# Optimization experiments

Hardware: AMD Instinct MI355X
Metric: run time of the kernel (lower is better)

## Reference

```python
import jax, jax.numpy as jnp
import numpy as np

N_NODES = 100000
N_EDGES = 100000
NNZ = 3200000
D_IN, D_HID, N_CLS = 512, 16, 7
NEG_SLOPE = 0.2


def _segment_softmax(scores, seg, num_segments, sorted_seg):
    m = jax.ops.segment_max(scores, seg, num_segments=num_segments,
                            indices_are_sorted=sorted_seg)
    ex = jnp.exp(scores - m[seg])
    s = jax.ops.segment_sum(ex, seg, num_segments=num_segments,
                            indices_are_sorted=sorted_seg)
    return ex / (s[seg] + 1e-9)


def _hypergat_layer(X, W, a1, a2, node_idx, edge_idx):
    # X: [N, din] -> h: [N, dout]
    h = X @ W
    hv = h[node_idx]                                   # [nnz, dout] gather
    # phase 1: node -> hyperedge attention (softmax within each hyperedge)
    s1 = jax.nn.leaky_relu(hv @ a1, NEG_SLOPE)         # [nnz]
    alpha = _segment_softmax(s1, edge_idx, N_EDGES, True)
    e = jax.ops.segment_sum(alpha[:, None] * hv, edge_idx,
                            num_segments=N_EDGES, indices_are_sorted=True)
    # phase 2: hyperedge -> node attention (softmax over edges incident to node)
    ev = e[edge_idx]                                   # [nnz, dout] gather
    s2 = jax.nn.leaky_relu(jnp.concatenate([hv, ev], axis=-1) @ a2, NEG_SLOPE)
    beta = _segment_softmax(s2, node_idx, N_NODES, False)
    out = jax.ops.segment_sum(beta[:, None] * ev, node_idx,
                              num_segments=N_NODES)
    return out


def setup_inputs() -> dict:
    key = jax.random.key(0)
    ks = jax.random.split(key, 8)
    H = jax.random.normal(ks[0], (N_NODES, D_IN), dtype=jnp.float32)
    node_idx = jax.random.randint(ks[1], (NNZ,), 0, N_NODES)
    edge_idx = jnp.sort(jax.random.randint(ks[2], (NNZ,), 0, N_EDGES))
    g1 = 1.0 / np.sqrt(D_IN)
    g2 = 1.0 / np.sqrt(D_HID)
    W1 = jax.random.uniform(ks[3], (D_IN, D_HID), jnp.float32, -g1, g1)
    a1_1 = jax.random.uniform(ks[4], (D_HID,), jnp.float32, -g2, g2)
    a2_1 = jax.random.uniform(ks[5], (2 * D_HID,), jnp.float32, -g2, g2)
    W2 = jax.random.uniform(ks[6], (D_HID, N_CLS), jnp.float32, -g2, g2)
    k7, k8 = jax.random.split(ks[7])
    gc = 1.0 / np.sqrt(N_CLS)
    a1_2 = jax.random.uniform(k7, (N_CLS,), jnp.float32, -gc, gc)
    a2_2 = jax.random.uniform(k8, (2 * N_CLS,), jnp.float32, -gc, gc)
    return {"H": H, "W1": W1, "a1_1": a1_1, "a2_1": a2_1,
            "W2": W2, "a1_2": a1_2, "a2_2": a2_2,
            "node_idx": node_idx, "edge_idx": edge_idx}


def reference(H, W1, a1_1, a2_1, W2, a1_2, a2_2, node_idx, edge_idx):
    H1 = _hypergat_layer(H, W1, a1_1, a2_1, node_idx, edge_idx)   # [N, 16]
    X2 = jax.nn.elu(H1)                                           # dropout off (eval)
    H2 = _hypergat_layer(X2, W2, a1_2, a2_2, node_idx, edge_idx)  # [N, 7]
    logp = jax.nn.log_softmax(H2, axis=1)
    return (logp, H1, H2)
```

## Files before the change

kernel.cpp:

```cpp
#include <hip/hip_runtime.h>
#include <hip/hip_bf16.h>
#include <math.h>

#define N_NODES 100000
#define N_EDGESC 100000
#define NNZ_C   3200000
#define D_IN    512
#define D_HID   16
#define N_CLS   7
#define NBK     782

#define G_GEMM 1563
#define G_HIST 1000
#define G_EOFF 3125
#define G_BIN  1000

typedef short short8 __attribute__((ext_vector_type(8)));
typedef float f32x4  __attribute__((ext_vector_type(4)));

__device__ __forceinline__ unsigned short f2bf_rn(float x) {
  unsigned int u = __float_as_uint(x);
  u += 0x7fff + ((u >> 16) & 1);
  return (unsigned short)(u >> 16);
}
__device__ __forceinline__ float bf2f(unsigned short b) {
  return __uint_as_float(((unsigned int)b) << 16);
}

__device__ __forceinline__ void eoff_body(int b, const int* __restrict__ eidx,
                                          int* __restrict__ eoff) {
  int i0 = (b * 256 + threadIdx.x) * 4;
  if (i0 >= NNZ_C) return;
  int4 v4 = *(const int4*)(eidx + i0);
  int vv[4] = {v4.x, v4.y, v4.z, v4.w};
  int prev = (i0 == 0) ? -1 : eidx[i0 - 1];
#pragma unroll
  for (int k = 0; k < 4; ++k) {
    for (int e = prev + 1; e <= vv[k]; ++e) eoff[e] = i0 + k;
    prev = vv[k];
  }
  if (i0 + 4 == NNZ_C) {
    for (int e = prev + 1; e <= N_EDGESC; ++e) eoff[e] = NNZ_C;
  }
}

__device__ __forceinline__ void hist_body(int b, const int* __restrict__ nidx,
                                          int* __restrict__ gcnt) {
  __shared__ int lh[NBK];
  int t = threadIdx.x;
  for (int i = t; i < NBK; i += 256) lh[i] = 0;
  __syncthreads();
  int base = b * 3200, end = base + 3200;
  for (int i = base + t; i < end; i += 256) atomicAdd(&lh[nidx[i] >> 7], 1);
  __syncthreads();
  for (int i = t; i < NBK; i += 256) {
    int c = lh[i];
    if (c) atomicAdd(&gcnt[i], c);
  }
}

__device__ __forceinline__ void bin_body(int b, const int* __restrict__ nidx,
                                         const int* __restrict__ eidx,
                                         int* __restrict__ bcur, int* __restrict__ binned) {
  __shared__ int lh[NBK];
  __shared__ int gb[NBK];
  int t = threadIdx.x;
  for (int i = t; i < NBK; i += 256) lh[i] = 0;
  __syncthreads();
  int base = b * 3200, end = base + 3200;
  for (int i = base + t; i < end; i += 256) atomicAdd(&lh[nidx[i] >> 7], 1);
  __syncthreads();
  for (int i = t; i < NBK; i += 256) {
    int c = lh[i];
    gb[i] = c ? atomicAdd(&bcur[i], c) : 0;
    lh[i] = 0;
  }
  __syncthreads();
  for (int i = base + t; i < end; i += 256) {
    int v = nidx[i], e = eidx[i];
    int bk = v >> 7;
    int r = atomicAdd(&lh[bk], 1);
    binned[gb[bk] + r] = e | ((v & 127) << 20);
  }
}

__global__ void bscan_kernel(const int* __restrict__ gcnt, int* __restrict__ boff,
                             int* __restrict__ bcur) {
  __shared__ int lds[1024];
  int t = threadIdx.x;
  int v = (t < NBK) ? gcnt[t] : 0;
  lds[t] = v;
  __syncthreads();
  for (int d = 1; d < 1024; d <<= 1) {
    int u = (t >= d) ? lds[t - d] : 0;
    __syncthreads();
    lds[t] += u;
    __syncthreads();
  }
  if (t < NBK) {
    boff[t + 1] = lds[t];
    bcur[t] = lds[t] - v;
  }
  if (t == 0) boff[0] = 0;
}

__global__ void csr_kernel(const int* __restrict__ binned, const int* __restrict__ boff,
                           int* __restrict__ noff, int* __restrict__ perm_e, int N) {
  __shared__ int lh[128];
  __shared__ int lsc[128];
  __shared__ int lcur[128];
  int b = blockIdx.x;
  int t = threadIdx.x;
  int s = boff[b], e = boff[b + 1];
  if (t < 128) lh[t] = 0;
  __syncthreads();
  for (int i = s + t; i < e; i += 256) {
    atomicAdd(&lh[binned[i] >> 20], 1);
  }
  __syncthreads();
  if (t < 128) lsc[t] = lh[t];
  __syncthreads();
  for (int d = 1; d < 128; d <<= 1) {
    int u = (t < 128 && t >= d) ? lsc[t - d] : 0;
    __syncthreads();
    if (t < 128) lsc[t] += u;
    __syncthreads();
  }
  if (t < 128) {
    int excl = lsc[t] - lh[t];
    lcur[t] = excl;
    int n = b * 128 + t;
    if (n <= N) noff[n] = s + excl;
  }
  __syncthreads();
  for (int i = s + t; i < e; i += 256) {
    int p = binned[i];
    int r = atomicAdd(&lcur[p >> 20], 1);
    perm_e[s + r] = p & 0xFFFFF;
  }
}

__device__ __forceinline__ void gemm1_body(int b,
    const float* __restrict__ X, const float* __restrict__ W,
    const float* __restrict__ a1, const float* __restrict__ a2,
    float* __restrict__ Hout, float2* __restrict__ phv) {
  int wid = b * 4 + (threadIdx.x >> 6);
  if (wid >= 6250) return;
  int lane = threadIdx.x & 63;
  int col  = lane & 15;
  int quad = lane >> 4;

  short8 wh[16], wl[16];
#pragma unroll
  for (int c = 0; c < 16; ++c) {
#pragma unroll
    for (int j = 0; j < 8; ++j) {
      float w = W[(c * 32 + quad * 8 + j) * 16 + col];
      unsigned short h = f2bf_rn(w);
      wh[c][j] = (short)h;
      wl[c][j] = (short)f2bf_rn(w - bf2f(h));
    }
  }

  int rowbase = wid * 16;
  const float4* Xr = (const float4*)(X + (size_t)(rowbase + col) * D_IN) + quad * 2;

  f32x4 acc_hh = {0.f, 0.f, 0.f, 0.f};
  f32x4 acc_hl = {0.f, 0.f, 0.f, 0.f};
  f32x4 acc_lh = {0.f, 0.f, 0.f, 0.f};

  float4 pre[4][2];
#pragma unroll
  for (int q = 0; q < 4; ++q) { pre[q][0] = Xr[q * 8]; pre[q][1] = Xr[q * 8 + 1]; }
#pragma unroll
  for (int c = 0; c < 16; ++c) {
    float4 u0 = pre[c & 3][0], u1 = pre[c & 3][1];
    if (c < 12) { pre[c & 3][0] = Xr[(c + 4) * 8]; pre[c & 3][1] = Xr[(c + 4) * 8 + 1]; }
    float xs[8] = {u0.x, u0.y, u0.z, u0.w, u1.x, u1.y, u1.z, u1.w};
    short8 ah, al;
#pragma unroll
    for (int j = 0; j < 8; ++j) {
      unsigned short h = f2bf_rn(xs[j]);
      ah[j] = (short)h;
      al[j] = (short)f2bf_rn(xs[j] - bf2f(h));
    }
    acc_hh = __builtin_amdgcn_mfma_f32_16x16x32_bf16(ah, wh[c], acc_hh, 0, 0, 0);
    acc_hl = __builtin_amdgcn_mfma_f32_16x16x32_bf16(ah, wl[c], acc_hl, 0, 0, 0);
    acc_lh = __builtin_amdgcn_mfma_f32_16x16x32_bf16(al, wh[c], acc_lh, 0, 0, 0);
  }

  float a1c = a1[col], a2c = a2[col];
#pragma unroll
  for (int r = 0; r < 4; ++r) {
    float v = acc_hh[r] + acc_hl[r] + acc_lh[r];
    int row = rowbase + quad * 4 + r;
    Hout[(size_t)row * 16 + col] = v;
    float p1 = v * a1c, p2 = v * a2c;
#pragma unroll
    for (int d = 1; d < 16; d <<= 1) { p1 += __shfl_xor(p1, d); p2 += __shfl_xor(p2, d); }
    if (col == 0) phv[row] = make_float2(p1, p2);
  }
}

__global__ __launch_bounds__(256) void k1_kernel(
    const float* __restrict__ X, const float* __restrict__ W1,
    const float* __restrict__ a1_1, const float* __restrict__ a2_1,
    float* __restrict__ Hout, float2* __restrict__ phv,
    const int* __restrict__ eidx, int* __restrict__ eoff,
    const int* __restrict__ nidx, int* __restrict__ gcnt) {
  int b = blockIdx.x;
  if (b < G_GEMM) {
    gemm1_body(b, X, W1, a1_1, a2_1, Hout, phv);
  } else if (b < G_GEMM + G_HIST) {
    hist_body(b - G_GEMM, nidx, gcnt);
  } else {
    eoff_body(b - G_GEMM - G_HIST, eidx, eoff);
  }
}

__device__ __forceinline__ void edge1_body(
    const float* __restrict__ h, const float2* __restrict__ phv,
    const float* __restrict__ a2, const int* __restrict__ eoff,
    const int* __restrict__ nidx, float* __restrict__ eout,
    float* __restrict__ pe, int wave, int lane) {
  if (wave >= N_EDGESC) return;
  int o0 = eoff[wave], o1 = eoff[wave + 1];
  int g = lane >> 4, t = lane & 15;
  if (o0 == o1) {
    if (g == 0) {
      eout[(size_t)wave * 16 + t] = 0.f;
      if (t == 0) pe[wave] = 0.f;
    }
    return;
  }
  float m = -1e30f, l = 0.f, acc = 0.f;
  for (int base = o0; base < o1; base += 64) {
    int nrem = o1 - base; if (nrem > 64) nrem = 64;
    int li = base + lane;
    int idx_l = nidx[li < o1 ? li : o1 - 1];
    for (int jb = 0; jb < nrem; jb += 16) {
      int j = jb + g;
      bool ok0 = j < nrem, ok1 = j + 4 < nrem, ok2 = j + 8 < nrem, ok3 = j + 12 < nrem;
      int v0 = __shfl(idx_l, j);
      int v1 = __shfl(idx_l, j + 4);
      int v2 = __shfl(idx_l, j + 8);
      int v3 = __shfl(idx_l, j + 12);
      float P0 = phv[v0].x, P1 = phv[v1].x, P2 = phv[v2].x, P3 = phv[v3].x;
      float h0 = h[(size_t)v0 * 16 + t];
      float h1 = h[(size_t)v1 * 16 + t];
      float h2 = h[(size_t)v2 * 16 + t];
      float h3 = h[(size_t)v3 * 16 + t];
      float s0 = ok0 ? (P0 > 0.f ? P0 : 0.2f * P0) : -1e30f;
      float s1 = ok1 ? (P1 > 0.f ? P1 : 0.2f * P1) : -1e30f;
      float s2 = ok2 ? (P2 > 0.f ? P2 : 0.2f * P2) : -1e30f;
      float s3 = ok3 ? (P3 > 0.f ? P3 : 0.2f * P3) : -1e30f;
      float mn = fmaxf(fmaxf(m, fmaxf(s0, s1)), fmaxf(s2, s3));
      float eo = __expf(m - mn);
      float e0 = ok0 ? __expf(s0 - mn) : 0.f;
      float e1 = ok1 ? __expf(s1 - mn) : 0.f;
      float e2 = ok2 ? __expf(s2 - mn) : 0.f;
      float e3 = ok3 ? __expf(s3 - mn) : 0.f;
      l = l * eo + ((e0 + e1) + (e2 + e3));
      acc = acc * eo + ((e0 * h0 + e1 * h1) + (e2 * h2 + e3 * h3));
      m = mn;
    }
  }
#pragma unroll
  for (int d = 16; d < 64; d <<= 1) {
    float mo = __shfl_xor(m, d), lo = __shfl_xor(l, d), ao = __shfl_xor(acc, d);
    float mn = fmaxf(m, mo);
    float ea = __expf(m - mn), eb = __expf(mo - mn);
    l = l * ea + lo * eb;
    acc = acc * ea + ao * eb;
    m = mn;
  }
  float val = acc / (l + 1e-9f);
  float pav = val * a2[16 + t];
#pragma unroll
  for (int d = 1; d < 16; d <<= 1) pav += __shfl_xor(pav, d);
  if (g == 0) {
    eout[(size_t)wave * 16 + t] = val;
    if (t == 0) pe[wave] = pav;
  }
}

__global__ __launch_bounds__(256) void k3_kernel(
    const int* __restrict__ nidx, const int* __restrict__ eidx,
    int* __restrict__ bcur, int* __restrict__ binned,
    const float* __restrict__ h1g, const float2* __restrict__ phv,
    const float* __restrict__ a2_1, const int* __restrict__ eoff,
    float* __restrict__ e1, float* __restrict__ pe) {
  int b = blockIdx.x;
  if (b < G_BIN) {
    bin_body(b, nidx, eidx, bcur, binned);
  } else {
    int wave = (b - G_BIN) * 4 + (threadIdx.x >> 6);
    edge1_body(h1g, phv, a2_1, eoff, nidx, e1, pe, wave, threadIdx.x & 63);
  }
}

__global__ __launch_bounds__(256) void node1_kernel(
    const float2* __restrict__ phv, const float* __restrict__ e1,
    const float* __restrict__ pe, const int* __restrict__ noff,
    const int* __restrict__ perm_e, float* __restrict__ H1out,
    float* __restrict__ h2g8, const float* __restrict__ W2,
    const float* __restrict__ a1_2, const float* __restrict__ a2_2,
    float* __restrict__ pn2) {
  int wave = (blockIdx.x * blockDim.x + threadIdx.x) >> 6;
  int lane = threadIdx.x & 63;
  if (wave >= N_NODES) return;
  int o0 = noff[wave], o1 = noff[wave + 1];
  int g = lane >> 4, t = lane & 15;
  float ph = phv[wave].y;
  float m = -1e30f, l = 0.f, acc = 0.f;
  for (int base = o0; base < o1; base += 64) {
    int nrem = o1 - base; if (nrem > 64) nrem = 64;
    int li = base + lane;
    int idx_l = perm_e[li < o1 ? li : o1 - 1];
    for (int jb = 0; jb < nrem; jb += 16) {
      int j = jb + g;
      bool ok0 = j < nrem, ok1 = j + 4 < nrem, ok2 = j + 8 < nrem, ok3 = j + 12 < nrem;
      int E0 = __shfl(idx_l, j);
      int E1 = __shfl(idx_l, j + 4);
      int E2 = __shfl(idx_l, j + 8);
      int E3 = __shfl(idx_l, j + 12);
      float P0 = ph + pe[E0], P1 = ph + pe[E1], P2 = ph + pe[E2], P3 = ph + pe[E3];
      float h0 = e1[(size_t)E0 * 16 + t];
      float h1 = e1[(size_t)E1 * 16 + t];
      float h2 = e1[(size_t)E2 * 16 + t];
      float h3 = e1[(size_t)E3 * 16 + t];
      float s0 = ok0 ? (P0 > 0.f ? P0 : 0.2f * P0) : -1e30f;
      float s1 = ok1 ? (P1 > 0.f ? P1 : 0.2f * P1) : -1e30f;
      float s2 = ok2 ? (P2 > 0.f ? P2 : 0.2f * P2) : -1e30f;
      float s3 = ok3 ? (P3 > 0.f ? P3 : 0.2f * P3) : -1e30f;
      float mn = fmaxf(fmaxf(m, fmaxf(s0, s1)), fmaxf(s2, s3));
      float eo = __expf(m - mn);
      float e0 = ok0 ? __expf(s0 - mn) : 0.f;
      float e1x = ok1 ? __expf(s1 - mn) : 0.f;
      float e2x = ok2 ? __expf(s2 - mn) : 0.f;
      float e3x = ok3 ? __expf(s3 - mn) : 0.f;
      l = l * eo + ((e0 + e1x) + (e2x + e3x));
      acc = acc * eo + ((e0 * h0 + e1x * h1) + (e2x * h2 + e3x * h3));
      m = mn;
    }
  }
#pragma unroll
  for (int d = 16; d < 64; d <<= 1) {
    float mo = __shfl_xor(m, d), lo = __shfl_xor(l, d), ao = __shfl_xor(acc, d);
    float ea_, eb_;
    float mn = fmaxf(m, mo);
    ea_ = __expf(m - mn); eb_ = __expf(mo - mn);
    l = l * ea_ + lo * eb_;
    acc = acc * ea_ + ao * eb_;
    m = mn;
  }
  float val = acc / (l + 1e-9f);
  if (g == 0) H1out[(size_t)wave * 16 + t] = val;
  float x = val > 0.f ? val : expm1f(val);
  float p1 = 0.f, p2s = 0.f, myh2 = 0.f;
#pragma unroll
  for (int j = 0; j < N_CLS; ++j) {
    float term = x * W2[t * N_CLS + j];
#pragma unroll
    for (int d = 1; d < 16; d <<= 1) term += __shfl_xor(term, d);
    p1 += term * a1_2[j];
    p2s += term * a2_2[j];
    if (t == j) myh2 = term;
  }
  if (g == 0) {
    if (t < N_CLS) h2g8[(size_t)wave * 8 + t] = myh2;
    if (t == 7) h2g8[(size_t)wave * 8 + 7] = p1;
    if (t == 0) pn2[wave] = p2s;
  }
}

__global__ __launch_bounds__(256) void edge2_kernel(
    const float* __restrict__ h2g8, const int* __restrict__ eoff,
    const int* __restrict__ nidx, const float* __restrict__ a2_2,
    float* __restrict__ e28) {
  int wave = (blockIdx.x * blockDim.x + threadIdx.x) >> 6;
  int lane = threadIdx.x & 63;
  if (wave >= N_EDGESC) return;
  int o0 = eoff[wave], o1 = eoff[wave + 1];
  int g = lane >> 3, t = lane & 7;
  if (o0 == o1) {
    if (g == 0) e28[(size_t)wave * 8 + t] = 0.f;
    return;
  }
  float m = -1e30f, l = 0.f, acc = 0.f;
  for (int base = o0; base < o1; base += 64) {
    int nrem = o1 - base; if (nrem > 64) nrem = 64;
    int li = base + lane;
    int idx_l = nidx[li < o1 ? li : o1 - 1];
    for (int jb = 0; jb < nrem; jb += 32) {
      int j = jb + g;
      bool ok0 = j < nrem, ok1 = j + 8 < nrem, ok2 = j + 16 < nrem, ok3 = j + 24 < nrem;
      int v0 = __shfl(idx_l, j);
      int v1 = __shfl(idx_l, j + 8);
      int v2 = __shfl(idx_l, j + 16);
      int v3 = __shfl(idx_l, j + 24);
      float f0 = h2g8[(size_t)v0 * 8 + t];
      float f1 = h2g8[(size_t)v1 * 8 + t];
      float f2 = h2g8[(size_t)v2 * 8 + t];
      float f3 = h2g8[(size_t)v3 * 8 + t];
      float P0 = __shfl(f0, lane | 7);
      float P1 = __shfl(f1, lane | 7);
      float P2 = __shfl(f2, lane | 7);
      float P3 = __shfl(f3, lane | 7);
      float h0 = (t < 7) ? f0 : 0.f;
      float h1 = (t < 7) ? f1 : 0.f;
      float h2v = (t < 7) ? f2 : 0.f;
      float h3 = (t < 7) ? f3 : 0.f;
      float s0 = ok0 ? (P0 > 0.f ? P0 : 0.2f * P0) : -1e30f;
      float s1 = ok1 ? (P1 > 0.f ? P1 : 0.2f * P1) : -1e30f;
      float s2 = ok2 ? (P2 > 0.f ? P2 : 0.2f * P2) : -1e30f;
      float s3 = ok3 ? (P3 > 0.f ? P3 : 0.2f * P3) : -1e30f;
      float mn = fmaxf(fmaxf(m, fmaxf(s0, s1)), fmaxf(s2, s3));
      float eo = __expf(m - mn);
      float e0 = ok0 ? __expf(s0 - mn) : 0.f;
      float e1 = ok1 ? __expf(s1 - mn) : 0.f;
      float e2 = ok2 ? __expf(s2 - mn) : 0.f;
      float e3 = ok3 ? __expf(s3 - mn) : 0.f;
      l = l * eo + ((e0 + e1) + (e2 + e3));
      acc = acc * eo + ((e0 * h0 + e1 * h1) + (e2 * h2v + e3 * h3));
      m = mn;
    }
  }
#pragma unroll
  for (int d = 8; d < 64; d <<= 1) {
    float mo = __shfl_xor(m, d), lo = __shfl_xor(l, d), ao = __shfl_xor(acc, d);
    float mn = fmaxf(m, mo);
    float ea = __expf(m - mn), eb = __expf(mo - mn);
    l = l * ea + lo * eb;
    acc = acc * ea + ao * eb;
    m = mn;
  }
  float val = acc / (l + 1e-9f);
  float pav = (t < 7) ? val * a2_2[7 + t] : 0.f;
#pragma unroll
  for (int d = 1; d < 8; d <<= 1) pav += __shfl_xor(pav, d);
  if (g == 0) e28[(size_t)wave * 8 + t] = (t < 7) ? val : pav;
}

__global__ __launch_bounds__(256) void node2_kernel(
    const float* __restrict__ e28, const float* __restrict__ pn2,
    const int* __restrict__ noff, const int* __restrict__ perm_e,
    float* __restrict__ H2out, float* __restrict__ logp) {
  int wave = (blockIdx.x * blockDim.x + threadIdx.x) >> 6;
  int lane = threadIdx.x & 63;
  if (wave >= N_NODES) return;
  int o0 = noff[wave], o1 = noff[wave + 1];
  int g = lane >> 3, t = lane & 7;
  float ph = pn2[wave];
  float m = -1e30f, l = 0.f, acc = 0.f;
  for (int base = o0; base < o1; base += 64) {
    int nrem = o1 - base; if (nrem > 64) nrem = 64;
    int li = base + lane;
    int idx_l = perm_e[li < o1 ? li : o1 - 1];
    for (int jb = 0; jb < nrem; jb += 32) {
      int j = jb + g;
      bool ok0 = j < nrem, ok1 = j + 8 < nrem, ok2 = j + 16 < nrem, ok3 = j + 24 < nrem;
      int E0 = __shfl(idx_l, j);
      int E1 = __shfl(idx_l, j + 8);
      int E2 = __shfl(idx_l, j + 16);
      int E3 = __shfl(idx_l, j + 24);
      float f0 = e28[(size_t)E0 * 8 + t];
      float f1 = e28[(size_t)E1 * 8 + t];
      float f2 = e28[(size_t)E2 * 8 + t];
      float f3 = e28[(size_t)E3 * 8 + t];
      float P0 = ph + __shfl(f0, lane | 7);
      float P1 = ph + __shfl(f1, lane | 7);
      float P2 = ph + __shfl(f2, lane | 7);
      float P3 = ph + __shfl(f3, lane | 7);
      float h0 = (t < 7) ? f0 : 0.f;
      float h1 = (t < 7) ? f1 : 0.f;
      float h2v = (t < 7) ? f2 : 0.f;
      float h3 = (t < 7) ? f3 : 0.f;
      float s0 = ok0 ? (P0 > 0.f ? P0 : 0.2f * P0) : -1e30f;
      float s1 = ok1 ? (P1 > 0.f ? P1 : 0.2f * P1) : -1e30f;
      float s2 = ok2 ? (P2 > 0.f ? P2 : 0.2f * P2) : -1e30f;
      float s3 = ok3 ? (P3 > 0.f ? P3 : 0.2f * P3) : -1e30f;
      float mn = fmaxf(fmaxf(m, fmaxf(s0, s1)), fmaxf(s2, s3));
      float eo = __expf(m - mn);
      float e0 = ok0 ? __expf(s0 - mn) : 0.f;
      float e1 = ok1 ? __expf(s1 - mn) : 0.f;
      float e2 = ok2 ? __expf(s2 - mn) : 0.f;
      float e3 = ok3 ? __expf(s3 - mn) : 0.f;
      l = l * eo + ((e0 + e1) + (e2 + e3));
      acc = acc * eo + ((e0 * h0 + e1 * h1) + (e2 * h2v + e3 * h3));
      m = mn;
    }
  }
#pragma unroll
  for (int d = 8; d < 64; d <<= 1) {
    float mo = __shfl_xor(m, d), lo = __shfl_xor(l, d), ao = __shfl_xor(acc, d);
    float mn = fmaxf(m, mo);
    float ea = __expf(m - mn), eb = __expf(mo - mn);
    l = l * ea + lo * eb;
    acc = acc * ea + ao * eb;
    m = mn;
  }
  float val = acc / (l + 1e-9f);
  if (g == 0 && t < 7) H2out[(size_t)wave * 7 + t] = val;
  float xm = (t < 7) ? val : -1e30f;
#pragma unroll
  for (int d = 1; d < 8; d <<= 1) xm = fmaxf(xm, __shfl_xor(xm, d));
  float se = (t < 7) ? __expf(val - xm) : 0.f;
#pragma unroll
  for (int d = 1; d < 8; d <<= 1) se += __shfl_xor(se, d);
  float lg = logf(se);
  if (g == 0 && t < 7) logp[(size_t)wave * 7 + t] = val - xm - lg;
}

extern "C" void kernel_launch(void* const* d_in, const int* in_sizes, int n_in,
                              void* d_out, int out_size, void* d_ws, size_t ws_size,
                              hipStream_t stream) {
  const float* H    = (const float*)d_in[0];
  const float* W1   = (const float*)d_in[1];
  const float* a1_1 = (const float*)d_in[2];
  const float* a2_1 = (const float*)d_in[3];
  const float* W2   = (const float*)d_in[4];
  const float* a1_2 = (const float*)d_in[5];
  const float* a2_2 = (const float*)d_in[6];
  const int* nidx   = (const int*)d_in[7];
  const int* eidx   = (const int*)d_in[8];

  float* outp = (float*)d_out;
  float* logp = outp;
  float* H1   = outp + (size_t)N_NODES * N_CLS;
  float* H2   = H1 + (size_t)N_NODES * D_HID;

  char* ws = (char*)d_ws;
  float* h1g  = (float*)(ws + 0);
  float* e1   = (float*)(ws + 6400000);
  float* h2g8 = (float*)(ws + 12800000);
  float* e28  = (float*)(ws + 16000000);
  int* eoff   = (int*)(ws + 19200000);
  int* noff   = (int*)(ws + 19600128);
  float* pe   = (float*)(ws + 20000256);
  float* pn2  = (float*)(ws + 20400256);
  float2* phv = (float2*)(ws + 20800256);
  int* perm_e = (int*)(ws + 21600256);
  int* gcnt   = (int*)(ws + 34400256);
  int* boff   = (int*)(ws + 34403456);
  int* bcur   = (int*)(ws + 34406656);
  int* binned = (int*)(ws + 34409856);

  const int TB = 256;

  hipMemsetAsync(gcnt, 0, NBK * sizeof(int), stream);
  k1_kernel<<<G_GEMM + G_HIST + G_EOFF, TB, 0, stream>>>(
      H, W1, a1_1, a2_1, h1g, phv, eidx, eoff, nidx, gcnt);
  bscan_kernel<<<1, 1024, 0, stream>>>(gcnt, boff, bcur);
  k3_kernel<<<G_BIN + 25000, TB, 0, stream>>>(
      nidx, eidx, bcur, binned, h1g, phv, a2_1, eoff, e1, pe);
  csr_kernel<<<NBK, TB, 0, stream>>>(binned, boff, noff, perm_e, N_NODES);
  node1_kernel<<<25000, TB, 0, stream>>>(phv, e1, pe, noff, perm_e, H1, h2g8,
                                         W2, a1_2, a2_2, pn2);
  edge2_kernel<<<25000, TB, 0, stream>>>(h2g8, eoff, nidx, a2_2, e28);
  node2_kernel<<<25000, TB, 0, stream>>>(e28, pn2, noff, perm_e, H2, logp);
}
```

Baseline: 622.5 us.

## Stage GEMM input tiles through double-buffered LDS and coarsen binning blocks

The first-layer GEMM now loads each block's 64x32 X slice cooperatively with coalesced row-contiguous float4 reads into a double-buffered shared-memory tile, instead of each lane striding across 16 separate rows. The aim is better global-load coalescing on the dominant 200MB X read. The cost is two barriers per k-step and shallower prefetch than the previous four-deep register pipeline. Separately, binning blocks each process 8x more edges (125 blocks), which cuts the number of global atomics on bucket cursors but leaves less parallelism.

```diff
diff --git a/kernel.cpp b/kernel.cpp
--- a/kernel.cpp
+++ b/kernel.cpp
@@ -13,7 +13,8 @@
 #define G_GEMM 1563
 #define G_HIST 1000
 #define G_EOFF 3125
-#define G_BIN  1000
+#define G_BIN  125
+#define BIN_PER 25600
 
 typedef short short8 __attribute__((ext_vector_type(8)));
 typedef float f32x4  __attribute__((ext_vector_type(4)));
@@ -67,7 +68,8 @@
   int t = threadIdx.x;
   for (int i = t; i < NBK; i += 256) lh[i] = 0;
   __syncthreads();
-  int base = b * 3200, end = base + 3200;
+  int base = b * BIN_PER, end = base + BIN_PER;
+  if (end > NNZ_C) end = NNZ_C;
   for (int i = base + t; i < end; i += 256) atomicAdd(&lh[nidx[i] >> 7], 1);
   __syncthreads();
   for (int i = t; i < NBK; i += 256) {
@@ -144,39 +146,56 @@
     const float* __restrict__ X, const float* __restrict__ W,
     const float* __restrict__ a1, const float* __restrict__ a2,
     float* __restrict__ Hout, float2* __restrict__ phv) {
-  int wid = b * 4 + (threadIdx.x >> 6);
-  if (wid >= 6250) return;
-  int lane = threadIdx.x & 63;
+  __shared__ __align__(16) float sX[2][8][256];
+  int tid  = threadIdx.x;
+  int w    = tid >> 6;
+  int lane = tid & 63;
   int col  = lane & 15;
   int quad = lane >> 4;
+  int row0 = b * 64;
 
   short8 wh[16], wl[16];
 #pragma unroll
   for (int c = 0; c < 16; ++c) {
 #pragma unroll
     for (int j = 0; j < 8; ++j) {
-      float w = W[(c * 32 + quad * 8 + j) * 16 + col];
-      unsigned short h = f2bf_rn(w);
+      float wv = W[(c * 32 + quad * 8 + j) * 16 + col];
+      unsigned short h = f2bf_rn(wv);
       wh[c][j] = (short)h;
-      wl[c][j] = (short)f2bf_rn(w - bf2f(h));
-    }
-  }
-
-  int rowbase = wid * 16;
-  const float4* Xr = (const float4*)(X + (size_t)(rowbase + col) * D_IN) + quad * 2;
+      wl[c][j] = (short)f2bf_rn(wv - bf2f(h));
+    }
+  }
+
+  int r0s = (tid >> 3), o0s = tid & 7;
+  int r1s = ((256 + tid) >> 3), o1s = tid & 7;
+  int rsrc0 = row0 + r0s; if (rsrc0 > N_NODES - 1) rsrc0 = N_NODES - 1;
+  int rsrc1 = row0 + r1s; if (rsrc1 > N_NODES - 1) rsrc1 = N_NODES - 1;
+  const float* src0 = X + (size_t)rsrc0 * D_IN + o0s * 4;
+  const float* src1 = X + (size_t)rsrc1 * D_IN + o1s * 4;
 
   f32x4 acc_hh = {0.f, 0.f, 0.f, 0.f};
   f32x4 acc_hl = {0.f, 0.f, 0.f, 0.f};
   f32x4 acc_lh = {0.f, 0.f, 0.f, 0.f};
 
-  float4 pre[4][2];
-#pragma unroll
-  for (int q = 0; q < 4; ++q) { pre[q][0] = Xr[q * 8]; pre[q][1] = Xr[q * 8 + 1]; }
+  int rl = (w << 4) + col;
+  int p0 = quad << 1, p1 = p0 + 1;
+
+  float4 va = *(const float4*)(src0);
+  float4 vb = *(const float4*)(src1);
+  *(float4*)&sX[0][o0s][r0s * 4] = va;
+  *(float4*)&sX[0][o1s][r1s * 4] = vb;
+
 #pragma unroll
   for (int c = 0; c < 16; ++c) {
-    float4 u0 = pre[c & 3][0], u1 = pre[c & 3][1];
-    if (c < 12) { pre[c & 3][0] = Xr[(c + 4) * 8]; pre[c & 3][1] = Xr[(c + 4) * 8 + 1]; }
-    float xs[8] = {u0.x, u0.y, u0.z, u0.w, u1.x, u1.y, u1.z, u1.w};
+    int cur = c & 1;
+    if (c < 15) {
+      va = *(const float4*)(src0 + (c + 1) * 32);
+      vb = *(const float4*)(src1 + (c + 1) * 32);
+    }
+    __syncthreads();
+    float4 f0 = *(const float4*)&sX[cur][p0][rl * 4];
+    float4 f1 = *(const float4*)&sX[cur][p1][rl * 4];
+    float xs[8] = {f0.x, f0.y, f0.z, f0.w, f1.x, f1.y, f1.z, f1.w};
     short8 ah, al;
 #pragma unroll
     for (int j = 0; j < 8; ++j) {
@@ -187,18 +206,27 @@
     acc_hh = __builtin_amdgcn_mfma_f32_16x16x32_bf16(ah, wh[c], acc_hh, 0, 0, 0);
     acc_hl = __builtin_amdgcn_mfma_f32_16x16x32_bf16(ah, wl[c], acc_hl, 0, 0, 0);
     acc_lh = __builtin_amdgcn_mfma_f32_16x16x32_bf16(al, wh[c], acc_lh, 0, 0, 0);
+    __syncthreads();
+    if (c < 15) {
+      int nb = (c + 1) & 1;
+      *(float4*)&sX[nb][o0s][r0s * 4] = va;
+      *(float4*)&sX[nb][o1s][r1s * 4] = vb;
+    }
   }
 
   float a1c = a1[col], a2c = a2[col];
+  int rowbase = row0 + w * 16;
 #pragma unroll
   for (int r = 0; r < 4; ++r) {
     float v = acc_hh[r] + acc_hl[r] + acc_lh[r];
     int row = rowbase + quad * 4 + r;
-    Hout[(size_t)row * 16 + col] = v;
-    float p1 = v * a1c, p2 = v * a2c;
-#pragma unroll
-    for (int d = 1; d < 16; d <<= 1) { p1 += __shfl_xor(p1, d); p2 += __shfl_xor(p2, d); }
-    if (col == 0) phv[row] = make_float2(p1, p2);
+    float p1e = v * a1c, p2e = v * a2c;
+#pragma unroll
+    for (int d = 1; d < 16; d <<= 1) { p1e += __shfl_xor(p1e, d); p2e += __shfl_xor(p2e, d); }
+    if (row < N_NODES) {
+      Hout[(size_t)row * 16 + col] = v;
+      if (col == 0) phv[row] = make_float2(p1e, p2e);
+    }
   }
 }
 
```

Result: faster. 597.4 us (-4.0%).

## Move binning to its own kernel and fuse CSR build with edge attention

Applied to the files above, without the earlier changes.

Binning of incidences by node bucket moves out of the fused edge-attention launch into a standalone kernel that uses fewer, larger blocks (12800 elements each instead of 3200). The CSR finalization kernel is then merged into the edge-attention launch, so the edge1 work now overlaps with CSR construction instead of with binning. The first fused kernel also reorders its block ranges so the histogram and edge-offset blocks are dispatched ahead of the GEMM blocks. The aim is to cut launch count and put the short dependent CSR stage alongside the long edge pass, at the cost of a serial bin launch with low parallelism.

```diff
diff --git a/kernel.cpp b/kernel.cpp
--- a/kernel.cpp
+++ b/kernel.cpp
@@ -10,10 +10,12 @@
 #define N_CLS   7
 #define NBK     782
 
-#define G_GEMM 1563
 #define G_HIST 1000
 #define G_EOFF 3125
-#define G_BIN  1000
+#define G_GEMM 1563
+#define G_BIN  250
+#define BIN_PER 12800
+#define G_CSR  NBK
 
 typedef short short8 __attribute__((ext_vector_type(8)));
 typedef float f32x4  __attribute__((ext_vector_type(4)));
@@ -56,87 +58,6 @@
   for (int i = t; i < NBK; i += 256) {
     int c = lh[i];
     if (c) atomicAdd(&gcnt[i], c);
-  }
-}
-
-__device__ __forceinline__ void bin_body(int b, const int* __restrict__ nidx,
-                                         const int* __restrict__ eidx,
-                                         int* __restrict__ bcur, int* __restrict__ binned) {
-  __shared__ int lh[NBK];
-  __shared__ int gb[NBK];
-  int t = threadIdx.x;
-  for (int i = t; i < NBK; i += 256) lh[i] = 0;
-  __syncthreads();
-  int base = b * 3200, end = base + 3200;
-  for (int i = base + t; i < end; i += 256) atomicAdd(&lh[nidx[i] >> 7], 1);
-  __syncthreads();
-  for (int i = t; i < NBK; i += 256) {
-    int c = lh[i];
-    gb[i] = c ? atomicAdd(&bcur[i], c) : 0;
-    lh[i] = 0;
-  }
-  __syncthreads();
-  for (int i = base + t; i < end; i += 256) {
-    int v = nidx[i], e = eidx[i];
-    int bk = v >> 7;
-    int r = atomicAdd(&lh[bk], 1);
-    binned[gb[bk] + r] = e | ((v & 127) << 20);
-  }
-}
-
-__global__ void bscan_kernel(const int* __restrict__ gcnt, int* __restrict__ boff,
-                             int* __restrict__ bcur) {
-  __shared__ int lds[1024];
-  int t = threadIdx.x;
-  int v = (t < NBK) ? gcnt[t] : 0;
-  lds[t] = v;
-  __syncthreads();
-  for (int d = 1; d < 1024; d <<= 1) {
-    int u = (t >= d) ? lds[t - d] : 0;
-    __syncthreads();
-    lds[t] += u;
-    __syncthreads();
-  }
-  if (t < NBK) {
-    boff[t + 1] = lds[t];
-    bcur[t] = lds[t] - v;
-  }
-  if (t == 0) boff[0] = 0;
-}
-
-__global__ void csr_kernel(const int* __restrict__ binned, const int* __restrict__ boff,
-                           int* __restrict__ noff, int* __restrict__ perm_e, int N) {
-  __shared__ int lh[128];
-  __shared__ int lsc[128];
-  __shared__ int lcur[128];
-  int b = blockIdx.x;
-  int t = threadIdx.x;
-  int s = boff[b], e = boff[b + 1];
-  if (t < 128) lh[t] = 0;
-  __syncthreads();
-  for (int i = s + t; i < e; i += 256) {
-    atomicAdd(&lh[binned[i] >> 20], 1);
-  }
-  __syncthreads();
-  if (t < 128) lsc[t] = lh[t];
-  __syncthreads();
-  for (int d = 1; d < 128; d <<= 1) {
-    int u = (t < 128 && t >= d) ? lsc[t - d] : 0;
-    __syncthreads();
-    if (t < 128) lsc[t] += u;
-    __syncthreads();
-  }
-  if (t < 128) {
-    int excl = lsc[t] - lh[t];
-    lcur[t] = excl;
-    int n = b * 128 + t;
-    if (n <= N) noff[n] = s + excl;
-  }
-  __syncthreads();
-  for (int i = s + t; i < e; i += 256) {
-    int p = binned[i];
-    int r = atomicAdd(&lcur[p >> 20], 1);
-    perm_e[s + r] = p & 0xFFFFF;
   }
 }
 
@@ -209,12 +130,96 @@
     const int* __restrict__ eidx, int* __restrict__ eoff,
     const int* __restrict__ nidx, int* __restrict__ gcnt) {
   int b = blockIdx.x;
-  if (b < G_GEMM) {
-    gemm1_body(b, X, W1, a1_1, a2_1, Hout, phv);
-  } else if (b < G_GEMM + G_HIST) {
-    hist_body(b - G_GEMM, nidx, gcnt);
+  if (b < G_HIST) {
+    hist_body(b, nidx, gcnt);
+  } else if (b < G_HIST + G_EOFF) {
+    eoff_body(b - G_HIST, eidx, eoff);
   } else {
-    eoff_body(b - G_GEMM - G_HIST, eidx, eoff);
+    gemm1_body(b - G_HIST - G_EOFF, X, W1, a1_1, a2_1, Hout, phv);
+  }
+}
+
+__global__ void bscan_kernel(const int* __restrict__ gcnt, int* __restrict__ boff,
+                             int* __restrict__ bcur) {
+  __shared__ int lds[1024];
+  int t = threadIdx.x;
+  int v = (t < NBK) ? gcnt[t] : 0;
+  lds[t] = v;
+  __syncthreads();
+  for (int d = 1; d < 1024; d <<= 1) {
+    int u = (t >= d) ? lds[t - d] : 0;
+    __syncthreads();
+    lds[t] += u;
+    __syncthreads();
+  }
+  if (t < NBK) {
+    boff[t + 1] = lds[t];
+    bcur[t] = lds[t] - v;
+  }
+  if (t == 0) boff[0] = 0;
+}
+
+__global__ __launch_bounds__(256) void bin_kernel(
+    const int* __restrict__ nidx, const int* __restrict__ eidx,
+    int* __restrict__ bcur, int* __restrict__ binned) {
+  __shared__ int lh[NBK];
+  __shared__ int gb[NBK];
+  int b = blockIdx.x;
+  int t = threadIdx.x;
+  for (int i = t; i < NBK; i += 256) lh[i] = 0;
+  __syncthreads();
+  int base = b * BIN_PER, end = base + BIN_PER;
+  if (end > NNZ_C) end = NNZ_C;
+  for (int i = base + t; i < end; i += 256) atomicAdd(&lh[nidx[i] >> 7], 1);
+  __syncthreads();
+  for (int i = t; i < NBK; i += 256) {
+    int c = lh[i];
+    gb[i] = c ? atomicAdd(&bcur[i], c) : 0;
+    lh[i] = 0;
+  }
+  __syncthreads();
+  for (int i = base + t; i < end; i += 256) {
+    int v = nidx[i], e = eidx[i];
+    int bk = v >> 7;
+    int r = atomicAdd(&lh[bk], 1);
+    binned[gb[bk] + r] = e | ((v & 127) << 20);
+  }
+}
+
+__device__ __forceinline__ void csr_body(int b, const int* __restrict__ binned,
+                                         const int* __restrict__ boff,
+                                         int* __restrict__ noff, int* __restrict__ perm_e,
+                                         int N) {
+  __shared__ int lh[128];
+  __shared__ int lsc[128];
+  __shared__ int lcur[128];
+  int t = threadIdx.x;
+  int s = boff[b], e = boff[b + 1];
+  if (t < 128) lh[t] = 0;
+  __syncthreads();
+  for (int i = s + t; i < e; i += 256) {
+    atomicAdd(&lh[binned[i] >> 20], 1);
+  }
+  __syncthreads();
+  if (t < 128) lsc[t] = lh[t];
+  __syncthreads();
+  for (int d = 1; d < 128; d <<= 1) {
+    int u = (t < 128 && t >= d) ? lsc[t - d] : 0;
+    __syncthreads();
+    if (t < 128) lsc[t] += u;
+    __syncthreads();
+  }
+  if (t < 128) {
+    int excl = lsc[t] - lh[t];
+    lcur[t] = excl;
+    int n = b * 128 + t;
+    if (n <= N) noff[n] = s + excl;
+  }
+  __syncthreads();
+  for (int i = s + t; i < e; i += 256) {
+    int p = binned[i];
+    int r = atomicAdd(&lcur[p >> 20], 1);
+    perm_e[s + r] = p & 0xFFFFF;
   }
 }
 
@@ -285,16 +290,16 @@
 }
 
 __global__ __launch_bounds__(256) void k3_kernel(
-    const int* __restrict__ nidx, const int* __restrict__ eidx,
-    int* __restrict__ bcur, int* __restrict__ binned,
+    const int* __restrict__ binned, const int* __restrict__ boff,
+    int* __restrict__ noff, int* __restrict__ perm_e,
     const float* __restrict__ h1g, const float2* __restrict__ phv,
     const float* __restrict__ a2_1, const int* __restrict__ eoff,
-    float* __restrict__ e1, float* __restrict__ pe) {
+    const int* __restrict__ nidx, float* __restrict__ e1, float* __restrict__ pe) {
   int b = blockIdx.x;
-  if (b < G_BIN) {
-    bin_body(b, nidx, eidx, bcur, binned);
+  if (b < G_CSR) {
+    csr_body(b, binned, boff, noff, perm_e, N_NODES);
   } else {
-    int wave = (b - G_BIN) * 4 + (threadIdx.x >> 6);
+    int wave = (b - G_CSR) * 4 + (threadIdx.x >> 6);
     edge1_body(h1g, phv, a2_1, eoff, nidx, e1, pe, wave, threadIdx.x & 63);
   }
 }
@@ -549,12 +554,12 @@
   const int TB = 256;
 
   hipMemsetAsync(gcnt, 0, NBK * sizeof(int), stream);
-  k1_kernel<<<G_GEMM + G_HIST + G_EOFF, TB, 0, stream>>>(
+  k1_kernel<<<G_HIST + G_EOFF + G_GEMM, TB, 0, stream>>>(
       H, W1, a1_1, a2_1, h1g, phv, eidx, eoff, nidx, gcnt);
   bscan_kernel<<<1, 1024, 0, stream>>>(gcnt, boff, bcur);
-  k3_kernel<<<G_BIN + 25000, TB, 0, stream>>>(
-      nidx, eidx, bcur, binned, h1g, phv, a2_1, eoff, e1, pe);
-  csr_kernel<<<NBK, TB, 0, stream>>>(binned, boff, noff, perm_e, N_NODES);
+  bin_kernel<<<G_BIN, TB, 0, stream>>>(nidx, eidx, bcur, binned);
+  k3_kernel<<<G_CSR + 25000, TB, 0, stream>>>(
+      binned, boff, noff, perm_e, h1g, phv, a2_1, eoff, nidx, e1, pe);
   node1_kernel<<<25000, TB, 0, stream>>>(phv, e1, pe, noff, perm_e, H1, h2g8,
                                          W2, a1_2, a2_2, pn2);
   edge2_kernel<<<25000, TB, 0, stream>>>(h2g8, eoff, nidx, a2_2, e28);
```

Result: no change. 622.3 us (-0.0%).
